# Kernel tuning notes

Hardware: AMD Instinct MI355X
Metric: run time of the kernel (lower is better)

The kernel has to match this reference:

```python
import jax, jax.numpy as jnp
import numpy as np

N = 100000
D = 64
FE = 8
E = 1600000


def setup_inputs() -> dict:
    key = jax.random.key(0)
    ks = jax.random.split(key, 24)
    s = 0.05
    inp = {
        "H_adapted_t": jax.random.normal(ks[0], (N, D), jnp.float32),
        "event_vector": jax.random.normal(ks[1], (N, FE), jnp.float32),
        "edge_index": jax.random.randint(ks[2], (2, E), 0, N, jnp.int32),
        # event encoder MLP
        "enc_W1": jax.random.normal(ks[3], (FE, D), jnp.float32) * s,
        "enc_b1": jnp.zeros((D,), jnp.float32),
        "enc_W2": jax.random.normal(ks[4], (D, D), jnp.float32) * s,
        "enc_b2": jnp.zeros((D,), jnp.float32),
        # GCNConv
        "gcn_W": jax.random.normal(ks[5], (D, D), jnp.float32) * s,
        "gcn_b": jnp.zeros((D,), jnp.float32),
        # GATConv (heads=1, concat=False)
        "gat_W": jax.random.normal(ks[6], (D, D), jnp.float32) * s,
        "gat_att_src": jax.random.normal(ks[7], (D,), jnp.float32) * s,
        "gat_att_dst": jax.random.normal(ks[8], (D,), jnp.float32) * s,
        "gat_b": jnp.zeros((D,), jnp.float32),
        # gate fusion
        "gate_W": jax.random.normal(ks[9], (2 * D, D), jnp.float32) * s,
        "gate_b": jnp.zeros((D,), jnp.float32),
        # residual decoder
        "res_W1": jax.random.normal(ks[10], (2 * D, D), jnp.float32) * s,
        "res_b1": jnp.zeros((D,), jnp.float32),
        "res_W2": jax.random.normal(ks[11], (D, D), jnp.float32) * s,
        "res_b2": jnp.zeros((D,), jnp.float32),
        # speed head
        "sp_W1": jax.random.normal(ks[12], (D, 32), jnp.float32) * s,
        "sp_b1": jnp.zeros((32,), jnp.float32),
        "sp_W2": jax.random.normal(ks[13], (32, 1), jnp.float32) * s,
        "sp_b2": jnp.zeros((1,), jnp.float32),
    }
    return inp


def _gcn(x, src, dst, W, b, n):
    # PyG GCNConv: x' = D^{-1/2} (A + I) D^{-1/2} X W + b
    h = x @ W
    deg = jax.ops.segment_sum(jnp.ones_like(dst, jnp.float32), dst, num_segments=n)
    dinv = jnp.where(deg > 0, jax.lax.rsqrt(jnp.maximum(deg, 1e-12)), 0.0)
    norm = dinv[src] * dinv[dst]  # [E+N]
    out = jax.ops.segment_sum(h[src] * norm[:, None], dst, num_segments=n)
    return out + b


def _gat(x, src, dst, W, att_src, att_dst, b, n):
    # PyG GATConv (1 head): alpha = softmax_dst(leaky_relu(a_s.Wx_src + a_d.Wx_dst))
    h = x @ W
    a_s = h @ att_src  # [n]
    a_d = h @ att_dst
    e = jax.nn.leaky_relu(a_s[src] + a_d[dst], negative_slope=0.2)  # [E+N]
    m = jax.ops.segment_max(e, dst, num_segments=n)
    ex = jnp.exp(e - m[dst])
    z = jax.ops.segment_sum(ex, dst, num_segments=n)
    alpha = ex / z[dst]
    out = jax.ops.segment_sum(h[src] * alpha[:, None], dst, num_segments=n)
    return out + b


def reference(H_adapted_t, event_vector, edge_index,
              enc_W1, enc_b1, enc_W2, enc_b2,
              gcn_W, gcn_b,
              gat_W, gat_att_src, gat_att_dst, gat_b,
              gate_W, gate_b,
              res_W1, res_b1, res_W2, res_b2,
              sp_W1, sp_b1, sp_W2, sp_b2):
    n = H_adapted_t.shape[0]
    # add self-loops (PyG default for both convs)
    loop = jnp.arange(n, dtype=edge_index.dtype)
    src = jnp.concatenate([edge_index[0], loop])
    dst = jnp.concatenate([edge_index[1], loop])

    # event encoder
    emb = jax.nn.relu(event_vector @ enc_W1 + enc_b1) @ enc_W2 + enc_b2
    # diffusion: GCN -> ReLU -> GAT -> ReLU
    x = jax.nn.relu(_gcn(emb, src, dst, gcn_W, gcn_b, n))
    diffused = jax.nn.relu(_gat(x, src, dst, gat_W, gat_att_src, gat_att_dst, gat_b, n))

    fusion = jnp.concatenate([H_adapted_t, diffused], axis=-1)  # [N, 2D]
    gate = jax.nn.sigmoid(fusion @ gate_W + gate_b)
    delta_raw = jax.nn.relu(fusion @ res_W1 + res_b1) @ res_W2 + res_b2
    delta = gate * delta_raw
    H_final = H_adapted_t + delta
    pred_speed = (jax.nn.relu(H_final @ sp_W1 + sp_b1) @ sp_W2 + sp_b2)[:, 0]
    return (delta, H_final, pred_speed)
```

## Files before the change

### kernel.cpp

```cpp
#include <hip/hip_runtime.h>
#include <hip/hip_bf16.h>

#define NN 100000
#define DD 64
#define FEE 8
#define EE 1600000

#define NBUCK 391
#define BCAP 6144
#define CHA 4096
#define NBLKA ((EE + CHA - 1) / CHA)

typedef __attribute__((ext_vector_type(8))) short bf16x8;
typedef __attribute__((ext_vector_type(4))) float f32x4;
typedef __attribute__((ext_vector_type(2))) float f32x2;

__device__ __forceinline__ float b2f(unsigned short u) {
    return __uint_as_float(((unsigned)u) << 16);
}
__device__ __forceinline__ unsigned short f2b(float f) {
    unsigned u = __float_as_uint(f);
    unsigned r = 0x7fffu + ((u >> 16) & 1u);
    return (unsigned short)((u + r) >> 16);
}
__device__ __forceinline__ float lrelu(float v) { return v > 0.f ? v : 0.2f * v; }
__device__ __forceinline__ unsigned fkey(float x) {
    unsigned b = __float_as_uint(x);
    return (b & 0x80000000u) ? ~b : (b | 0x80000000u);
}
__device__ __forceinline__ float funkey(unsigned u) {
    unsigned b = (u & 0x80000000u) ? (u & 0x7fffffffu) : ~u;
    return __uint_as_float(b);
}
__device__ __forceinline__ int rdlane(int v, int l) {
    return __builtin_amdgcn_readlane(v, l);
}
__device__ __forceinline__ float rdlanef(float v, int l) {
    return __int_as_float(__builtin_amdgcn_readlane(__float_as_int(v), l));
}
__device__ __forceinline__ bf16x8 pack8(const float* p) {
    const float4 a = *(const float4*)p;
    const float4 b = *(const float4*)(p + 4);
    bf16x8 r;
    r[0] = (short)f2b(a.x); r[1] = (short)f2b(a.y);
    r[2] = (short)f2b(a.z); r[3] = (short)f2b(a.w);
    r[4] = (short)f2b(b.x); r[5] = (short)f2b(b.y);
    r[6] = (short)f2b(b.z); r[7] = (short)f2b(b.w);
    return r;
}

__device__ __forceinline__ float deq8(unsigned v) {
#if __has_builtin(__builtin_amdgcn_cvt_f32_fp8)
    return __builtin_amdgcn_cvt_f32_fp8(v & 0xffu, 0);
#else
    unsigned t = v & 0x7fu;
    float m = __uint_as_float(0x3C000000u + (t << 20));
    if (t < 8) m = 2.f * m - 0.015625f;
    return (v & 0x80u) ? -m : m;
#endif
}
__device__ __forceinline__ float4 deq8x4(unsigned v) {
#if __has_builtin(__builtin_amdgcn_cvt_pk_f32_fp8)
    f32x2 lo = __builtin_amdgcn_cvt_pk_f32_fp8((int)v, false);
    f32x2 hi = __builtin_amdgcn_cvt_pk_f32_fp8((int)v, true);
    return make_float4(lo[0], lo[1], hi[0], hi[1]);
#else
    return make_float4(deq8(v), deq8(v >> 8), deq8(v >> 16), deq8(v >> 24));
#endif
}
__device__ __forceinline__ unsigned q8(float f) {
    unsigned u = __float_as_uint(f);
    unsigned s = (u >> 24) & 0x80u;
    float a = fminf(__uint_as_float(u & 0x7fffffffu), 448.f);
    unsigned t;
    if (a < 0.015625f) {
        t = (unsigned)__float2int_rn(a * 512.f);
    } else {
        unsigned b = __float_as_uint(a);
        b += ((b >> 20) & 1u) + 0x7FFFFu;
        unsigned e = (b >> 23) - 120u;
        t = (e > 15u) ? 0x7Eu : (((b >> 20) & 7u) | (e << 3));
    }
    return s | t;
}
__device__ __forceinline__ unsigned pk4(float a, float b, float c, float d) {
    return q8(a) | (q8(b) << 8) | (q8(c) << 16) | (q8(d) << 24);
}

#define LK 136
#define LK2 72

__global__ __launch_bounds__(256, 4) void k_encoder_mfma(
    const float* __restrict__ ev, const float* __restrict__ W1, const float* __restrict__ b1,
    const float* __restrict__ W2, const float* __restrict__ b2,
    const float* __restrict__ gcnW, const float* __restrict__ dinv,
    unsigned char* __restrict__ hA8)
{
    __shared__ short sW1T[64 * 32];
    __shared__ short sW2T[64 * LK2];
    __shared__ short sGWT[64 * LK2];
    __shared__ float sb1[64], sb2[64];
    __shared__ short sStage[4][16 * LK2];

    for (int t = threadIdx.x; t < 64 * 32; t += 256) {
        int n = t >> 5, k = t & 31;
        sW1T[n * 32 + k] = (k < FEE) ? (short)f2b(W1[k * 64 + n]) : (short)0;
    }
    for (int t = threadIdx.x; t < 64 * 64; t += 256) {
        int k = t >> 6, n = t & 63;
        sW2T[n * LK2 + k] = (short)f2b(W2[t]);
        sGWT[n * LK2 + k] = (short)f2b(gcnW[t]);
    }
    if (threadIdx.x < 64) {
        sb1[threadIdx.x] = b1[threadIdx.x];
        sb2[threadIdx.x] = b2[threadIdx.x];
    }
    __syncthreads();

    const int wave = threadIdx.x >> 6;
    const int lane = threadIdx.x & 63;
    const int m16  = lane & 15;
    const int quad = lane >> 4;
    short* myStage = &sStage[wave][0];

    const int ngroups = NN / 16;
    for (int g = blockIdx.x * 4 + wave; g < ngroups; g += gridDim.x * 4) {
        const int row0 = g * 16;
        bf16x8 a0;
        #pragma unroll
        for (int i = 0; i < 8; i++) a0[i] = 0;
        if (quad == 0) a0 = pack8(ev + (size_t)(row0 + m16) * FEE);
        f32x4 acc[4];
        #pragma unroll
        for (int c = 0; c < 4; c++) {
            f32x4 z = {0.f, 0.f, 0.f, 0.f};
            acc[c] = __builtin_amdgcn_mfma_f32_16x16x32_bf16(
                a0, *(const bf16x8*)&sW1T[(c * 16 + m16) * 32 + quad * 8], z, 0, 0, 0);
        }
        #pragma unroll
        for (int c = 0; c < 4; c++) {
            int n = c * 16 + m16;
            float bb = sb1[n];
            #pragma unroll
            for (int r = 0; r < 4; r++)
                myStage[(quad * 4 + r) * LK2 + n] = (short)f2b(fmaxf(acc[c][r] + bb, 0.f));
        }
        bf16x8 af0 = *(const bf16x8*)&myStage[m16 * LK2 + quad * 8];
        bf16x8 af1 = *(const bf16x8*)&myStage[m16 * LK2 + 32 + quad * 8];
        #pragma unroll
        for (int c = 0; c < 4; c++) {
            f32x4 z = {0.f, 0.f, 0.f, 0.f};
            const short* bp = &sW2T[(c * 16 + m16) * LK2 + quad * 8];
            z = __builtin_amdgcn_mfma_f32_16x16x32_bf16(af0, *(const bf16x8*)bp, z, 0, 0, 0);
            acc[c] = __builtin_amdgcn_mfma_f32_16x16x32_bf16(af1, *(const bf16x8*)(bp + 32), z, 0, 0, 0);
        }
        #pragma unroll
        for (int c = 0; c < 4; c++) {
            int n = c * 16 + m16;
            float bb = sb2[n];
            #pragma unroll
            for (int r = 0; r < 4; r++)
                myStage[(quad * 4 + r) * LK2 + n] = (short)f2b(acc[c][r] + bb);
        }
        af0 = *(const bf16x8*)&myStage[m16 * LK2 + quad * 8];
        af1 = *(const bf16x8*)&myStage[m16 * LK2 + 32 + quad * 8];
        #pragma unroll
        for (int c = 0; c < 4; c++) {
            f32x4 z = {0.f, 0.f, 0.f, 0.f};
            const short* bp = &sGWT[(c * 16 + m16) * LK2 + quad * 8];
            z = __builtin_amdgcn_mfma_f32_16x16x32_bf16(af0, *(const bf16x8*)bp, z, 0, 0, 0);
            acc[c] = __builtin_amdgcn_mfma_f32_16x16x32_bf16(af1, *(const bf16x8*)(bp + 32), z, 0, 0, 0);
        }
        #pragma unroll
        for (int c = 0; c < 4; c++) {
            int n = c * 16 + m16;
            #pragma unroll
            for (int r = 0; r < 4; r++)
                myStage[(quad * 4 + r) * LK2 + n] = (short)f2b(acc[c][r]);
        }
        #pragma unroll
        for (int h = 0; h < 2; h++) {
            int row = h * 8 + (lane >> 3);
            int col = (lane & 7) * 8;
            float sc = 32.f * dinv[row0 + row];
            const short* sp = &myStage[row * LK2 + col];
            uint2 w;
            w.x = pk4(b2f(sp[0]) * sc, b2f(sp[1]) * sc, b2f(sp[2]) * sc, b2f(sp[3]) * sc);
            w.y = pk4(b2f(sp[4]) * sc, b2f(sp[5]) * sc, b2f(sp[6]) * sc, b2f(sp[7]) * sc);
            *(uint2*)(hA8 + (size_t)(row0 + row) * 64 + col) = w;
        }
    }
}

__global__ __launch_bounds__(256, 4) void k_gatw_mfma(
    const unsigned short* __restrict__ x, const float* __restrict__ gatW,
    const float* __restrict__ attS, const float* __restrict__ attD,
    unsigned char* __restrict__ hC8, float* __restrict__ a_s, float* __restrict__ a_d)
{
    __shared__ short sGWT[64 * LK2];
    __shared__ float sAS[64], sAD[64];
    __shared__ short sStage[4][16 * LK2];
    for (int t = threadIdx.x; t < 64 * 64; t += 256) {
        int k = t >> 6, n = t & 63;
        sGWT[n * LK2 + k] = (short)f2b(gatW[t]);
    }
    if (threadIdx.x < 64) {
        sAS[threadIdx.x] = attS[threadIdx.x];
        sAD[threadIdx.x] = attD[threadIdx.x];
    }
    __syncthreads();

    const int wave = threadIdx.x >> 6;
    const int lane = threadIdx.x & 63;
    const int m16  = lane & 15;
    const int quad = lane >> 4;
    short* myStage = &sStage[wave][0];

    const int ngroups = NN / 16;
    for (int g = blockIdx.x * 4 + wave; g < ngroups; g += gridDim.x * 4) {
        const int row0 = g * 16;
        const unsigned short* xr = x + (size_t)(row0 + m16) * 64 + quad * 8;
        bf16x8 af0 = *(const bf16x8*)xr;
        bf16x8 af1 = *(const bf16x8*)(xr + 32);
        f32x4 acc[4];
        #pragma unroll
        for (int c = 0; c < 4; c++) {
            f32x4 z = {0.f, 0.f, 0.f, 0.f};
            const short* bp = &sGWT[(c * 16 + m16) * LK2 + quad * 8];
            z = __builtin_amdgcn_mfma_f32_16x16x32_bf16(af0, *(const bf16x8*)bp, z, 0, 0, 0);
            acc[c] = __builtin_amdgcn_mfma_f32_16x16x32_bf16(af1, *(const bf16x8*)(bp + 32), z, 0, 0, 0);
        }
        float ps[4] = {0.f, 0.f, 0.f, 0.f}, pd[4] = {0.f, 0.f, 0.f, 0.f};
        #pragma unroll
        for (int c = 0; c < 4; c++) {
            int n = c * 16 + m16;
            float was = sAS[n], wad = sAD[n];
            #pragma unroll
            for (int r = 0; r < 4; r++) {
                float v = acc[c][r];
                myStage[(quad * 4 + r) * LK2 + n] = (short)f2b(v);
                ps[r] += v * was;
                pd[r] += v * wad;
            }
        }
        #pragma unroll
        for (int off = 1; off < 16; off <<= 1) {
            #pragma unroll
            for (int r = 0; r < 4; r++) {
                ps[r] += __shfl_xor(ps[r], off, 64);
                pd[r] += __shfl_xor(pd[r], off, 64);
            }
        }
        if (m16 == 0) {
            #pragma unroll
            for (int r = 0; r < 4; r++) {
                a_s[row0 + quad * 4 + r] = ps[r];
                a_d[row0 + quad * 4 + r] = pd[r];
            }
        }
        #pragma unroll
        for (int h = 0; h < 2; h++) {
            int row = h * 8 + (lane >> 3);
            int col = (lane & 7) * 8;
            const short* sp = &myStage[row * LK2 + col];
            uint2 w;
            w.x = pk4(b2f(sp[0]) * 32.f, b2f(sp[1]) * 32.f, b2f(sp[2]) * 32.f, b2f(sp[3]) * 32.f);
            w.y = pk4(b2f(sp[4]) * 32.f, b2f(sp[5]) * 32.f, b2f(sp[6]) * 32.f, b2f(sp[7]) * 32.f);
            *(uint2*)(hC8 + (size_t)(row0 + row) * 64 + col) = w;
        }
    }
}

__global__ __launch_bounds__(512, 4) void k_decoder_mfma(
    const float* __restrict__ H, const float* diff,
    const float* __restrict__ gateW, const float* __restrict__ gateB,
    const float* __restrict__ resW1, const float* __restrict__ resB1,
    const float* __restrict__ resW2, const float* __restrict__ resB2,
    const float* __restrict__ spW1, const float* __restrict__ spB1,
    const float* __restrict__ spW2, const float* __restrict__ spB2,
    float* outDelta, float* __restrict__ outH, float* __restrict__ outP)
{
    __shared__ short sGW[64 * LK];
    __shared__ short sRW1[64 * LK];
    __shared__ short sRW2[64 * LK2];
    __shared__ short sSW1[32 * LK2];
    __shared__ float sGB[64], sRB1[64], sRB2[64];
    __shared__ float sSB1[32], sSW2[32];
    __shared__ float sSB2;
    __shared__ short sStage[8][16 * LK2];

    for (int t = threadIdx.x; t < 128 * 64; t += 512) {
        int k = t >> 6, n = t & 63;
        sGW[n * LK + k]  = (short)f2b(gateW[t]);
        sRW1[n * LK + k] = (short)f2b(resW1[t]);
    }
    for (int t = threadIdx.x; t < 64 * 64; t += 512) {
        int k = t >> 6, n = t & 63;
        sRW2[n * LK2 + k] = (short)f2b(resW2[t]);
    }
    for (int t = threadIdx.x; t < 64 * 32; t += 512) {
        int k = t >> 5, n = t & 31;
        sSW1[n * LK2 + k] = (short)f2b(spW1[t]);
    }
    if (threadIdx.x < 64) {
        sGB[threadIdx.x]  = gateB[threadIdx.x];
        sRB1[threadIdx.x] = resB1[threadIdx.x];
        sRB2[threadIdx.x] = resB2[threadIdx.x];
    }
    if (threadIdx.x < 32) {
        sSB1[threadIdx.x] = spB1[threadIdx.x];
        sSW2[threadIdx.x] = spW2[threadIdx.x];
    }
    if (threadIdx.x == 0) sSB2 = spB2[0];
    __syncthreads();

    const int wave = threadIdx.x >> 6;
    const int lane = threadIdx.x & 63;
    const int m16  = lane & 15;
    const int quad = lane >> 4;
    short* myStage = &sStage[wave][0];

    const int ngroups = NN / 16;
    for (int g = blockIdx.x * 8 + wave; g < ngroups; g += gridDim.x * 8) {
        const int row0 = g * 16;
        const float* Hrow = H    + (size_t)(row0 + m16) * 64 + quad * 8;
        const float* Drow = diff + (size_t)(row0 + m16) * 64 + quad * 8;
        bf16x8 afrag[4];
        afrag[0] = pack8(Hrow);
        afrag[1] = pack8(Hrow + 32);
        afrag[2] = pack8(Drow);
        afrag[3] = pack8(Drow + 32);

        f32x4 accG[4], accR[4];
        #pragma unroll
        for (int c = 0; c < 4; c++) {
            f32x4 z = {0.f, 0.f, 0.f, 0.f};
            accG[c] = z; accR[c] = z;
        }
        #pragma unroll
        for (int c = 0; c < 4; c++) {
            const short* bg = &sGW[(c * 16 + m16) * LK + quad * 8];
            const short* br = &sRW1[(c * 16 + m16) * LK + quad * 8];
            #pragma unroll
            for (int t = 0; t < 4; t++) {
                bf16x8 bgf = *(const bf16x8*)(bg + 32 * t);
                accG[c] = __builtin_amdgcn_mfma_f32_16x16x32_bf16(afrag[t], bgf, accG[c], 0, 0, 0);
                bf16x8 brf = *(const bf16x8*)(br + 32 * t);
                accR[c] = __builtin_amdgcn_mfma_f32_16x16x32_bf16(afrag[t], brf, accR[c], 0, 0, 0);
            }
        }

        float gateV[4][4];
        #pragma unroll
        for (int c = 0; c < 4; c++) {
            int n = c * 16 + m16;
            float gb = sGB[n], rb = sRB1[n];
            #pragma unroll
            for (int r = 0; r < 4; r++) {
                gateV[c][r] = 1.f / (1.f + __expf(-(accG[c][r] + gb)));
                int mrow = quad * 4 + r;
                myStage[mrow * LK2 + n] = (short)f2b(fmaxf(accR[c][r] + rb, 0.f));
            }
        }
        bf16x8 h1f0 = *(const bf16x8*)&myStage[m16 * LK2 + quad * 8];
        bf16x8 h1f1 = *(const bf16x8*)&myStage[m16 * LK2 + 32 + quad * 8];

        f32x4 accD[4];
        #pragma unroll
        for (int c = 0; c < 4; c++) { f32x4 z = {0.f, 0.f, 0.f, 0.f}; accD[c] = z; }
        #pragma unroll
        for (int c = 0; c < 4; c++) {
            const short* bp = &sRW2[(c * 16 + m16) * LK2 + quad * 8];
            accD[c] = __builtin_amdgcn_mfma_f32_16x16x32_bf16(h1f0, *(const bf16x8*)bp, accD[c], 0, 0, 0);
            accD[c] = __builtin_amdgcn_mfma_f32_16x16x32_bf16(h1f1, *(const bf16x8*)(bp + 32), accD[c], 0, 0, 0);
        }

        #pragma unroll
        for (int c = 0; c < 4; c++) {
            int n = c * 16 + m16;
            float rb2 = sRB2[n];
            #pragma unroll
            for (int r = 0; r < 4; r++) {
                int mrow = quad * 4 + r;
                float delta = gateV[c][r] * (accD[c][r] + rb2);
                float hv = H[(size_t)(row0 + mrow) * 64 + n];
                float hf = hv + delta;
                outDelta[(size_t)(row0 + mrow) * 64 + n] = delta;
                outH[(size_t)(row0 + mrow) * 64 + n] = hf;
                myStage[mrow * LK2 + n] = (short)f2b(hf);
            }
        }
        bf16x8 hff0 = *(const bf16x8*)&myStage[m16 * LK2 + quad * 8];
        bf16x8 hff1 = *(const bf16x8*)&myStage[m16 * LK2 + 32 + quad * 8];

        f32x4 accS[2];
        { f32x4 z = {0.f, 0.f, 0.f, 0.f}; accS[0] = z; accS[1] = z; }
        #pragma unroll
        for (int c = 0; c < 2; c++) {
            const short* bp = &sSW1[(c * 16 + m16) * LK2 + quad * 8];
            accS[c] = __builtin_amdgcn_mfma_f32_16x16x32_bf16(hff0, *(const bf16x8*)bp, accS[c], 0, 0, 0);
            accS[c] = __builtin_amdgcn_mfma_f32_16x16x32_bf16(hff1, *(const bf16x8*)(bp + 32), accS[c], 0, 0, 0);
        }
        float part[4];
        #pragma unroll
        for (int r = 0; r < 4; r++) {
            float p0 = fmaxf(accS[0][r] + sSB1[m16], 0.f) * sSW2[m16];
            float p1 = fmaxf(accS[1][r] + sSB1[16 + m16], 0.f) * sSW2[16 + m16];
            part[r] = p0 + p1;
        }
        #pragma unroll
        for (int off = 1; off < 16; off <<= 1) {
            #pragma unroll
            for (int r = 0; r < 4; r++) part[r] += __shfl_xor(part[r], off, 64);
        }
        if (m16 == 0) {
            #pragma unroll
            for (int r = 0; r < 4; r++) outP[row0 + quad * 4 + r] = part[r] + sSB2;
        }
    }
}


__global__ __launch_bounds__(256, 2) void k_binA(
    const int* __restrict__ src, const int* __restrict__ dst,
    int* __restrict__ bcnt, int* __restrict__ bpacked)
{
    __shared__ int sCount[512];
    __shared__ int sOff[512];
    __shared__ int sCur[512];
    __shared__ int sGbase[512];
    __shared__ int sScan[256];
    __shared__ int sStage[CHA];
    __shared__ unsigned short sBkt[CHA];
    const int t = threadIdx.x;
    const int e0 = blockIdx.x * CHA;
    const int len = min(CHA, EE - e0);

    for (int i = t; i < 512; i += 256) sCount[i] = 0;
    __syncthreads();
    for (int i = t; i < len; i += 256) atomicAdd(&sCount[dst[e0 + i] >> 8], 1);
    __syncthreads();
    int a0 = sCount[2 * t], a1 = sCount[2 * t + 1];
    int pairsum = a0 + a1;
    sScan[t] = pairsum;
    __syncthreads();
    for (int off = 1; off < 256; off <<= 1) {
        int v = (t >= off) ? sScan[t - off] : 0;
        __syncthreads();
        sScan[t] += v;
        __syncthreads();
    }
    int excl = sScan[t] - pairsum;
    sOff[2 * t] = excl;       sOff[2 * t + 1] = excl + a0;
    sCur[2 * t] = excl;       sCur[2 * t + 1] = excl + a0;
    __syncthreads();
    for (int b = t; b < NBUCK; b += 256) {
        int c = sCount[b];
        sGbase[b] = c ? atomicAdd(&bcnt[b], c) : 0;
    }
    __syncthreads();
    for (int i = t; i < len; i += 256) {
        int d = dst[e0 + i];
        int s = src[e0 + i];
        int b = d >> 8;
        int p = atomicAdd(&sCur[b], 1);
        sStage[p] = ((d & 255) << 17) | s;
        sBkt[p] = (unsigned short)b;
    }
    __syncthreads();
    for (int i = t; i < len; i += 256) {
        int b = sBkt[i];
        int gp = sGbase[b] + (i - sOff[b]);
        if (gp < BCAP) bpacked[(size_t)b * BCAP + gp] = sStage[i];
    }
}

__global__ __launch_bounds__(256) void k_fillB2(
    const int* __restrict__ bcnt, const int* __restrict__ bpacked,
    int* __restrict__ row_ptr, int* __restrict__ rend, float* __restrict__ dinv,
    int* __restrict__ csr)
{
    __shared__ int lcnt[256];
    __shared__ int lscan[256];
    __shared__ int lcur[256];
    __shared__ int lstage[BCAP];
    __shared__ int sWs[4];
    __shared__ int sBase;
    const int b = blockIdx.x;
    const int t = threadIdx.x;
    const int node0 = b << 8;
    const int cnt = min(bcnt[b], BCAP);
    lcnt[t] = 0;
    int partial = 0;
    for (int i = t; i < b; i += 256) partial += bcnt[i];
    #pragma unroll
    for (int o = 32; o >= 1; o >>= 1) partial += __shfl_xor(partial, o, 64);
    if ((t & 63) == 0) sWs[t >> 6] = partial;
    __syncthreads();
    if (t == 0) sBase = sWs[0] + sWs[1] + sWs[2] + sWs[3];
    const int* bp = bpacked + (size_t)b * BCAP;
    for (int i = t; i < cnt; i += 256) atomicAdd(&lcnt[bp[i] >> 17], 1);
    __syncthreads();
    const int base = sBase;
    int own = lcnt[t];
    lscan[t] = own;
    __syncthreads();
    for (int off = 1; off < 256; off <<= 1) {
        int v = (t >= off) ? lscan[t - off] : 0;
        __syncthreads();
        lscan[t] += v;
        __syncthreads();
    }
    int excl = lscan[t] - own;
    int node = node0 + t;
    if (node < NN) {
        row_ptr[node] = base + excl;
        rend[node] = base + excl + own;
        dinv[node] = rsqrtf((float)own + 1.0f);
    }
    lcur[t] = excl;
    __syncthreads();
    for (int i = t; i < cnt; i += 256) {
        int v = bp[i];
        int p = atomicAdd(&lcur[v >> 17], 1);
        lstage[p] = v & 0x1FFFF;
    }
    __syncthreads();
    for (int i = t; i < cnt; i += 256) csr[base + i] = lstage[i];
}


__global__ __launch_bounds__(256) void k_gcn_gather(
    const int* __restrict__ row_ptr, const int* __restrict__ rend,
    const int* __restrict__ csr, const float* __restrict__ dinv,
    const unsigned char* __restrict__ hA8, const float* __restrict__ gcnB,
    unsigned short* __restrict__ x)
{
    const int slot = threadIdx.x >> 6;
    const int lane = threadIdx.x & 63;
    const int g    = lane >> 4;
    const int c4   = (lane & 15) * 4;
    const float4 gb = *(const float4*)(gcnB + c4);
    const int stride = gridDim.x * 4;
    for (int node = blockIdx.x * 4 + slot; node < NN; node += stride) {
        const int base = row_ptr[node], end = rend[node];
        float r0 = 0.f, r1 = 0.f, r2 = 0.f, r3 = 0.f;
        for (int cb = base; cb < end; cb += 64) {
            int rem = end - cb; if (rem > 64) rem = 64;
            int sidx = (lane < rem) ? csr[cb + lane] : 0;
            int k = 0;
            for (; k + 16 <= rem; k += 16) {
                #pragma unroll
                for (int u = 0; u < 4; u++) {
                    int s = __shfl(sidx, k + u * 4 + g, 64);
                    unsigned v = *(const unsigned*)(hA8 + (((unsigned)s << 6) | (unsigned)c4));
                    float4 d = deq8x4(v);
                    r0 += d.x; r1 += d.y; r2 += d.z; r3 += d.w;
                }
            }
            for (; k < rem; k += 4) {
                int kk = k + g;
                int kc = min(kk, rem - 1);
                int s = __shfl(sidx, kc, 64);
                float w = (kk < rem) ? 1.f : 0.f;
                unsigned v = *(const unsigned*)(hA8 + (((unsigned)s << 6) | (unsigned)c4));
                float4 d = deq8x4(v);
                r0 = fmaf(d.x, w, r0); r1 = fmaf(d.y, w, r1);
                r2 = fmaf(d.z, w, r2); r3 = fmaf(d.w, w, r3);
            }
        }
        r0 += __shfl_xor(r0, 16, 64); r0 += __shfl_xor(r0, 32, 64);
        r1 += __shfl_xor(r1, 16, 64); r1 += __shfl_xor(r1, 32, 64);
        r2 += __shfl_xor(r2, 16, 64); r2 += __shfl_xor(r2, 32, 64);
        r3 += __shfl_xor(r3, 16, 64); r3 += __shfl_xor(r3, 32, 64);
        unsigned sv = *(const unsigned*)(hA8 + (((unsigned)node << 6) | (unsigned)c4));
        float4 sd = deq8x4(sv);
        float sc = dinv[node] * 0.03125f;
        if (g == 0) {
            float o0 = fmaxf(fmaf(r0 + sd.x, sc, gb.x), 0.f);
            float o1 = fmaxf(fmaf(r1 + sd.y, sc, gb.y), 0.f);
            float o2 = fmaxf(fmaf(r2 + sd.z, sc, gb.z), 0.f);
            float o3 = fmaxf(fmaf(r3 + sd.w, sc, gb.w), 0.f);
            uint2 wv;
            wv.x = (unsigned)f2b(o0) | ((unsigned)f2b(o1) << 16);
            wv.y = (unsigned)f2b(o2) | ((unsigned)f2b(o3) << 16);
            *(uint2*)(x + (size_t)node * 64 + c4) = wv;
        }
    }
}

__global__ __launch_bounds__(256) void k_gat_fused(
    const int* __restrict__ row_ptr, const int* __restrict__ rend,
    const int* __restrict__ csr,
    const float* __restrict__ a_s, const float* __restrict__ a_d,
    const unsigned char* __restrict__ hC8, const float* __restrict__ gatB,
    float* __restrict__ diff)
{
    const int slot = threadIdx.x >> 6;
    const int lane = threadIdx.x & 63;
    const int g    = lane >> 4;
    const int c4   = (lane & 15) * 4;
    const float4 gb = *(const float4*)(gatB + c4);
    const int stride = gridDim.x * 4;
    for (int node = blockIdx.x * 4 + slot; node < NN; node += stride) {
        const int base = row_ptr[node], end = rend[node];
        const float adn = a_d[node];
        const float p0 = __expf(lrelu(a_s[node] + adn));
        float z = p0;
        float r0 = 0.f, r1 = 0.f, r2 = 0.f, r3 = 0.f;
        for (int cb = base; cb < end; cb += 64) {
            int rem = end - cb; if (rem > 64) rem = 64;
            int sidx = 0; float p = 0.f;
            if (lane < rem) {
                sidx = csr[cb + lane];
                p = __expf(lrelu(a_s[sidx] + adn));
            }
            float pzs = p;
            #pragma unroll
            for (int o = 32; o >= 1; o >>= 1) pzs += __shfl_xor(pzs, o, 64);
            z += pzs;
            int k = 0;
            for (; k + 16 <= rem; k += 16) {
                #pragma unroll
                for (int u = 0; u < 4; u++) {
                    int kk = k + u * 4 + g;
                    int s = __shfl(sidx, kk, 64);
                    float w = __shfl(p, kk, 64);
                    unsigned v = *(const unsigned*)(hC8 + (((unsigned)s << 6) | (unsigned)c4));
                    float4 d = deq8x4(v);
                    r0 = fmaf(d.x, w, r0); r1 = fmaf(d.y, w, r1);
                    r2 = fmaf(d.z, w, r2); r3 = fmaf(d.w, w, r3);
                }
            }
            for (; k < rem; k += 4) {
                int kk = k + g;
                int kc = min(kk, rem - 1);
                int s = __shfl(sidx, kc, 64);
                float w = __shfl(p, kc, 64);
                if (kk >= rem) w = 0.f;
                unsigned v = *(const unsigned*)(hC8 + (((unsigned)s << 6) | (unsigned)c4));
                float4 d = deq8x4(v);
                r0 = fmaf(d.x, w, r0); r1 = fmaf(d.y, w, r1);
                r2 = fmaf(d.z, w, r2); r3 = fmaf(d.w, w, r3);
            }
        }
        r0 += __shfl_xor(r0, 16, 64); r0 += __shfl_xor(r0, 32, 64);
        r1 += __shfl_xor(r1, 16, 64); r1 += __shfl_xor(r1, 32, 64);
        r2 += __shfl_xor(r2, 16, 64); r2 += __shfl_xor(r2, 32, 64);
        r3 += __shfl_xor(r3, 16, 64); r3 += __shfl_xor(r3, 32, 64);
        unsigned sv = *(const unsigned*)(hC8 + (((unsigned)node << 6) | (unsigned)c4));
        float4 sd = deq8x4(sv);
        r0 = fmaf(sd.x, p0, r0); r1 = fmaf(sd.y, p0, r1);
        r2 = fmaf(sd.z, p0, r2); r3 = fmaf(sd.w, p0, r3);
        if (g == 0) {
            float inv = 1.f / (32.f * z);
            float4 ov;
            ov.x = fmaxf(fmaf(r0, inv, gb.x), 0.f);
            ov.y = fmaxf(fmaf(r1, inv, gb.y), 0.f);
            ov.z = fmaxf(fmaf(r2, inv, gb.z), 0.f);
            ov.w = fmaxf(fmaf(r3, inv, gb.w), 0.f);
            *(float4*)(diff + (size_t)node * 64 + c4) = ov;
        }
    }
}


__global__ __launch_bounds__(256, 4) void k_encoder(
    const float* __restrict__ ev, const float* __restrict__ W1, const float* __restrict__ b1,
    const float* __restrict__ W2, const float* __restrict__ b2,
    const float* __restrict__ gcnW, unsigned short* __restrict__ hA)
{
    __shared__ float sW1[FEE * DD];
    __shared__ float sW2[DD * DD];
    __shared__ float sGW[DD * DD];
    __shared__ float sb1[DD], sb2[DD];
    __shared__ float stage[4 * DD];
    for (int t = threadIdx.x; t < FEE * DD; t += 256) sW1[t] = W1[t];
    for (int t = threadIdx.x; t < DD * DD; t += 256) sW2[t] = W2[t];
    for (int t = threadIdx.x; t < DD * DD; t += 256) sGW[t] = gcnW[t];
    if (threadIdx.x < DD) {
        sb1[threadIdx.x] = b1[threadIdx.x];
        sb2[threadIdx.x] = b2[threadIdx.x];
    }
    __syncthreads();
    const int slot = threadIdx.x >> 6, j = threadIdx.x & 63;
    const int ngroups = NN / 4;
    for (int g = blockIdx.x; g < ngroups; g += gridDim.x) {
        int node = g * 4 + slot;
        const float* evp = ev + node * FEE;
        float accv = sb1[j];
        #pragma unroll
        for (int i = 0; i < FEE; i++) accv += evp[i] * sW1[i * DD + j];
        float hid = fmaxf(accv, 0.f);
        stage[slot * DD + j] = hid;
        __syncthreads();
        float embv = sb2[j];
        #pragma unroll 8
        for (int i = 0; i < DD; i++) embv += stage[slot * DD + i] * sW2[i * DD + j];
        __syncthreads();
        stage[slot * DD + j] = embv;
        __syncthreads();
        float hv = 0.f;
        #pragma unroll 8
        for (int i = 0; i < DD; i++) hv += stage[slot * DD + i] * sGW[i * DD + j];
        hA[node * DD + j] = f2b(hv);
        __syncthreads();
    }
}

__global__ void k_degf(const int* __restrict__ dst, float* __restrict__ deg) {
    int e = blockIdx.x * 256 + threadIdx.x;
    if (e < EE) atomicAdd(&deg[dst[e]], 1.0f);
}
__global__ void k_dinvf(float* deg) {
    int i = blockIdx.x * 256 + threadIdx.x;
    if (i < NN) deg[i] = rsqrtf(deg[i] + 1.0f);
}
__global__ __launch_bounds__(256) void k_gcn_agg(
    const int* __restrict__ src, const int* __restrict__ dst,
    const float* __restrict__ dinv, const unsigned short* __restrict__ hA,
    float* __restrict__ acc)
{
    int lane = threadIdx.x & 63;
    int w = blockIdx.x * 4 + (threadIdx.x >> 6);
    int nw = gridDim.x * 4;
    for (int e = w; e < EE; e += nw) {
        int s = src[e], d = dst[e];
        float norm = dinv[s] * dinv[d];
        atomicAdd(&acc[d * DD + lane], b2f(hA[s * DD + lane]) * norm);
    }
}
__global__ __launch_bounds__(256, 4) void k_gcn_post(
    const float* __restrict__ acc, const unsigned short* __restrict__ hA,
    const float* __restrict__ dinv, const float* __restrict__ gcnB,
    const float* __restrict__ gatW, const float* __restrict__ attS, const float* __restrict__ attD,
    unsigned short* __restrict__ hC, float* __restrict__ a_s, float* __restrict__ a_d,
    unsigned int* __restrict__ mkey)
{
    __shared__ float sGW[DD * DD];
    __shared__ float sB[DD], sAS[DD], sAD[DD];
    __shared__ float stage[4 * DD];
    for (int t = threadIdx.x; t < DD * DD; t += 256) sGW[t] = gatW[t];
    if (threadIdx.x < DD) {
        sB[threadIdx.x] = gcnB[threadIdx.x];
        sAS[threadIdx.x] = attS[threadIdx.x];
        sAD[threadIdx.x] = attD[threadIdx.x];
    }
    __syncthreads();
    const int slot = threadIdx.x >> 6, j = threadIdx.x & 63;
    const int ngroups = NN / 4;
    for (int g = blockIdx.x; g < ngroups; g += gridDim.x) {
        int node = g * 4 + slot;
        float dv = dinv[node];
        float xv = fmaxf(acc[node * DD + j] + b2f(hA[node * DD + j]) * dv * dv + sB[j], 0.f);
        stage[slot * DD + j] = xv;
        __syncthreads();
        float hv = 0.f;
        #pragma unroll 8
        for (int i = 0; i < DD; i++) hv += stage[slot * DD + i] * sGW[i * DD + j];
        hC[node * DD + j] = f2b(hv);
        float ts = hv * sAS[j], td = hv * sAD[j];
        #pragma unroll
        for (int m = 32; m >= 1; m >>= 1) {
            ts += __shfl_xor(ts, m, 64);
            td += __shfl_xor(td, m, 64);
        }
        if (j == 0) {
            a_s[node] = ts;
            a_d[node] = td;
            mkey[node] = fkey(lrelu(ts + td));
        }
        __syncthreads();
    }
}
__global__ void k_gat_max(const int* __restrict__ src, const int* __restrict__ dst,
                          const float* __restrict__ a_s, const float* __restrict__ a_d,
                          unsigned int* __restrict__ mkey) {
    int e = blockIdx.x * 256 + threadIdx.x;
    if (e < EE) {
        int d = dst[e];
        float v = lrelu(a_s[src[e]] + a_d[d]);
        atomicMax(&mkey[d], fkey(v));
    }
}
__global__ void k_gat_mz(const float* __restrict__ a_s, const float* __restrict__ a_d,
                         unsigned int* __restrict__ mkey, float* __restrict__ z) {
    int i = blockIdx.x * 256 + threadIdx.x;
    if (i < NN) {
        float m = funkey(mkey[i]);
        float es = lrelu(a_s[i] + a_d[i]);
        z[i] = expf(es - m);
        ((float*)mkey)[i] = m;
    }
}
__global__ void k_gat_z(const int* __restrict__ src, const int* __restrict__ dst,
                        const float* __restrict__ a_s, const float* __restrict__ a_d,
                        const float* __restrict__ mf, float* __restrict__ z) {
    int e = blockIdx.x * 256 + threadIdx.x;
    if (e < EE) {
        int d = dst[e];
        float v = lrelu(a_s[src[e]] + a_d[d]);
        atomicAdd(&z[d], expf(v - mf[d]));
    }
}
__global__ __launch_bounds__(256) void k_gat_agg(
    const int* __restrict__ src, const int* __restrict__ dst,
    const float* __restrict__ a_s, const float* __restrict__ a_d,
    const float* __restrict__ mf, const float* __restrict__ z,
    const unsigned short* __restrict__ hC, float* __restrict__ acc)
{
    int lane = threadIdx.x & 63;
    int w = blockIdx.x * 4 + (threadIdx.x >> 6);
    int nw = gridDim.x * 4;
    for (int e = w; e < EE; e += nw) {
        int s = src[e], d = dst[e];
        float v = lrelu(a_s[s] + a_d[d]);
        float alpha = expf(v - mf[d]) / z[d];
        atomicAdd(&acc[d * DD + lane], b2f(hC[s * DD + lane]) * alpha);
    }
}
__global__ void k_gat_post(float* __restrict__ acc, const unsigned short* __restrict__ hC,
                           const float* __restrict__ a_s, const float* __restrict__ a_d,
                           const float* __restrict__ mf, const float* __restrict__ z,
                           const float* __restrict__ gatB) {
    int idx = blockIdx.x * 256 + threadIdx.x;
    if (idx < NN * DD) {
        int i = idx >> 6, j = idx & 63;
        float es = lrelu(a_s[i] + a_d[i]);
        float sw = expf(es - mf[i]) / z[i];
        float v = acc[idx] + sw * b2f(hC[idx]) + gatB[j];
        acc[idx] = fmaxf(v, 0.f);
    }
}


extern "C" void kernel_launch(void* const* d_in, const int* in_sizes, int n_in,
                              void* d_out, int out_size, void* d_ws, size_t ws_size,
                              hipStream_t stream) {
    const float* H     = (const float*)d_in[0];
    const float* ev    = (const float*)d_in[1];
    const int*   ei    = (const int*)d_in[2];
    const float* encW1 = (const float*)d_in[3];
    const float* encB1 = (const float*)d_in[4];
    const float* encW2 = (const float*)d_in[5];
    const float* encB2 = (const float*)d_in[6];
    const float* gcnW  = (const float*)d_in[7];
    const float* gcnB  = (const float*)d_in[8];
    const float* gatW  = (const float*)d_in[9];
    const float* attS  = (const float*)d_in[10];
    const float* attD  = (const float*)d_in[11];
    const float* gatB  = (const float*)d_in[12];
    const float* gateW = (const float*)d_in[13];
    const float* gateB = (const float*)d_in[14];
    const float* resW1 = (const float*)d_in[15];
    const float* resB1 = (const float*)d_in[16];
    const float* resW2 = (const float*)d_in[17];
    const float* resB2 = (const float*)d_in[18];
    const float* spW1  = (const float*)d_in[19];
    const float* spB1  = (const float*)d_in[20];
    const float* spW2  = (const float*)d_in[21];
    const float* spB2  = (const float*)d_in[22];

    const int* srcI = ei;
    const int* dstI = ei + EE;

    float* outDelta = (float*)d_out;
    float* outH     = outDelta + (size_t)NN * DD;
    float* outP     = outH + (size_t)NN * DD;

    float* diff = outDelta;
    int* bpacked = (int*)outDelta;
    unsigned short* x   = (unsigned short*)outDelta;
    unsigned char* hA8  = (unsigned char*)outH;
    unsigned char* hC8  = hA8 + (size_t)NN * DD;

    const size_t csr_need = ((size_t)4 * NN + EE + 1024) * 4;

    if (ws_size >= csr_need) {
        float* dinv = (float*)d_ws;
        float* a_s  = dinv + NN;
        float* a_d  = a_s + NN;
        int* rend   = (int*)(a_d + NN);
        int* csr    = rend + NN;
        int* bcntg  = csr + EE;
        int* row_ptr = (int*)outP;

        hipMemsetAsync(bcntg, 0, (size_t)512 * 4, stream);
        k_binA<<<NBLKA, 256, 0, stream>>>(srcI, dstI, bcntg, bpacked);
        k_fillB2<<<NBUCK, 256, 0, stream>>>(bcntg, bpacked,
                                            row_ptr, rend, dinv, csr);
        k_encoder_mfma<<<1024, 256, 0, stream>>>(ev, encW1, encB1, encW2, encB2,
                                                 gcnW, dinv, hA8);
        k_gcn_gather<<<4096, 256, 0, stream>>>(row_ptr, rend, csr, dinv, hA8, gcnB, x);
        k_gatw_mfma<<<1024, 256, 0, stream>>>(x, gatW, attS, attD, hC8, a_s, a_d);
        k_gat_fused<<<4096, 256, 0, stream>>>(row_ptr, rend, csr, a_s, a_d, hC8, gatB, diff);
    } else {
        float* dinv = (float*)d_ws;
        float* a_s  = dinv + NN;
        float* a_d  = a_s + NN;
        float* mf   = a_d + NN;
        float* z    = mf + NN;
        float* acc  = diff;
        unsigned short* hA = (unsigned short*)outH;
        unsigned short* hC = hA + (size_t)NN * DD;

        hipMemsetAsync(dinv, 0, (size_t)NN * 4, stream);
        hipMemsetAsync(acc, 0, (size_t)NN * DD * 4, stream);
        k_encoder<<<1024, 256, 0, stream>>>(ev, encW1, encB1, encW2, encB2, gcnW, hA);
        k_degf<<<(EE + 255) / 256, 256, 0, stream>>>(dstI, dinv);
        k_dinvf<<<(NN + 255) / 256, 256, 0, stream>>>(dinv);
        k_gcn_agg<<<8192, 256, 0, stream>>>(srcI, dstI, dinv, hA, acc);
        k_gcn_post<<<1024, 256, 0, stream>>>(acc, hA, dinv, gcnB, gatW, attS, attD,
                                             hC, a_s, a_d, (unsigned int*)mf);
        hipMemsetAsync(acc, 0, (size_t)NN * DD * 4, stream);
        k_gat_max<<<(EE + 255) / 256, 256, 0, stream>>>(srcI, dstI, a_s, a_d, (unsigned int*)mf);
        k_gat_mz<<<(NN + 255) / 256, 256, 0, stream>>>(a_s, a_d, (unsigned int*)mf, z);
        k_gat_z<<<(EE + 255) / 256, 256, 0, stream>>>(srcI, dstI, a_s, a_d, mf, z);
        k_gat_agg<<<8192, 256, 0, stream>>>(srcI, dstI, a_s, a_d, mf, z, hC, acc);
        k_gat_post<<<(NN * DD) / 256, 256, 0, stream>>>(acc, hC, a_s, a_d, mf, z, gatB);
    }

    k_decoder_mfma<<<512, 512, 0, stream>>>(H, diff, gateW, gateB, resW1, resB1,
                                            resW2, resB2, spW1, spB1, spW2, spB2,
                                            outDelta, outH, outP);
}
```

Measured before the change: 284.6 us.

## Process two nodes per wave in GCN/GAT gathers with LDS-staged edge lists

Each 64-lane wave now handles two destination nodes, one per 32-lane half, instead of one node across four 16-lane groups. Edge source indices and weights are staged in per-half shared memory rather than broadcast with shuffles. The gather loop first issues 8 independent row loads, then dequantizes and accumulates them, to raise memory-level parallelism. The cost is more registers and LDS traffic, plus unsynchronized LDS reuse within a half-wave, which relies on wave-lockstep execution.

Result: faster. 262.0 us (-7.9%).

```diff
diff --git a/kernel.cpp b/kernel.cpp
--- a/kernel.cpp
+++ b/kernel.cpp
@@ -31,12 +31,6 @@
 __device__ __forceinline__ float funkey(unsigned u) {
     unsigned b = (u & 0x80000000u) ? (u & 0x7fffffffu) : ~u;
     return __uint_as_float(b);
-}
-__device__ __forceinline__ int rdlane(int v, int l) {
-    return __builtin_amdgcn_readlane(v, l);
-}
-__device__ __forceinline__ float rdlanef(float v, int l) {
-    return __int_as_float(__builtin_amdgcn_readlane(__float_as_int(v), l));
 }
 __device__ __forceinline__ bf16x8 pack8(const float* p) {
     const float4 a = *(const float4*)p;
@@ -536,47 +530,62 @@
     const unsigned char* __restrict__ hA8, const float* __restrict__ gcnB,
     unsigned short* __restrict__ x)
 {
-    const int slot = threadIdx.x >> 6;
+    __shared__ int2 sE[4][2][32];
+    const int wave = threadIdx.x >> 6;
     const int lane = threadIdx.x & 63;
-    const int g    = lane >> 4;
+    const int half = lane >> 5;
+    const int hl   = lane & 31;
+    const int g2   = hl >> 4;
     const int c4   = (lane & 15) * 4;
+    int2* myE = sE[wave][half];
     const float4 gb = *(const float4*)(gcnB + c4);
-    const int stride = gridDim.x * 4;
-    for (int node = blockIdx.x * 4 + slot; node < NN; node += stride) {
+    const int stride = gridDim.x * 8;
+    for (int node = blockIdx.x * 8 + wave * 2 + half; node < NN; node += stride) {
         const int base = row_ptr[node], end = rend[node];
         float r0 = 0.f, r1 = 0.f, r2 = 0.f, r3 = 0.f;
-        for (int cb = base; cb < end; cb += 64) {
-            int rem = end - cb; if (rem > 64) rem = 64;
-            int sidx = (lane < rem) ? csr[cb + lane] : 0;
+        for (int cb = base; cb < end; cb += 32) {
+            int rem = end - cb; if (rem > 32) rem = 32;
+            int sidx = 0; float w = 0.f;
+            if (hl < rem) { sidx = csr[cb + hl]; w = 1.f; }
+            myE[hl] = make_int2(sidx, __float_as_int(w));
             int k = 0;
             for (; k + 16 <= rem; k += 16) {
+                unsigned vv[8]; float ww[8];
                 #pragma unroll
-                for (int u = 0; u < 4; u++) {
-                    int s = __shfl(sidx, k + u * 4 + g, 64);
-                    unsigned v = *(const unsigned*)(hA8 + (((unsigned)s << 6) | (unsigned)c4));
-                    float4 d = deq8x4(v);
-                    r0 += d.x; r1 += d.y; r2 += d.z; r3 += d.w;
+                for (int j = 0; j < 8; j++) {
+                    int2 e = myE[k + 2 * j + g2];
+                    ww[j] = __int_as_float(e.y);
+                    vv[j] = *(const unsigned*)(hA8 + (((unsigned)e.x << 6) | (unsigned)c4));
                 }
-            }
-            for (; k < rem; k += 4) {
-                int kk = k + g;
-                int kc = min(kk, rem - 1);
-                int s = __shfl(sidx, kc, 64);
-                float w = (kk < rem) ? 1.f : 0.f;
-                unsigned v = *(const unsigned*)(hA8 + (((unsigned)s << 6) | (unsigned)c4));
-                float4 d = deq8x4(v);
-                r0 = fmaf(d.x, w, r0); r1 = fmaf(d.y, w, r1);
-                r2 = fmaf(d.z, w, r2); r3 = fmaf(d.w, w, r3);
-            }
-        }
-        r0 += __shfl_xor(r0, 16, 64); r0 += __shfl_xor(r0, 32, 64);
-        r1 += __shfl_xor(r1, 16, 64); r1 += __shfl_xor(r1, 32, 64);
-        r2 += __shfl_xor(r2, 16, 64); r2 += __shfl_xor(r2, 32, 64);
-        r3 += __shfl_xor(r3, 16, 64); r3 += __shfl_xor(r3, 32, 64);
+                #pragma unroll
+                for (int j = 0; j < 8; j++) {
+                    float4 d = deq8x4(vv[j]);
+                    r0 = fmaf(d.x, ww[j], r0); r1 = fmaf(d.y, ww[j], r1);
+                    r2 = fmaf(d.z, ww[j], r2); r3 = fmaf(d.w, ww[j], r3);
+                }
+            }
+            for (; k < rem; k += 8) {
+                unsigned vv[4]; float ww[4];
+                #pragma unroll
+                for (int j = 0; j < 4; j++) {
+                    int2 e = myE[k + 2 * j + g2];
+                    ww[j] = __int_as_float(e.y);
+                    vv[j] = *(const unsigned*)(hA8 + (((unsigned)e.x << 6) | (unsigned)c4));
+                }
+                #pragma unroll
+                for (int j = 0; j < 4; j++) {
+                    float4 d = deq8x4(vv[j]);
+                    r0 = fmaf(d.x, ww[j], r0); r1 = fmaf(d.y, ww[j], r1);
+                    r2 = fmaf(d.z, ww[j], r2); r3 = fmaf(d.w, ww[j], r3);
+                }
+            }
+        }
+        r0 += __shfl_xor(r0, 16, 64); r1 += __shfl_xor(r1, 16, 64);
+        r2 += __shfl_xor(r2, 16, 64); r3 += __shfl_xor(r3, 16, 64);
         unsigned sv = *(const unsigned*)(hA8 + (((unsigned)node << 6) | (unsigned)c4));
         float4 sd = deq8x4(sv);
         float sc = dinv[node] * 0.03125f;
-        if (g == 0) {
+        if (g2 == 0) {
             float o0 = fmaxf(fmaf(r0 + sd.x, sc, gb.x), 0.f);
             float o1 = fmaxf(fmaf(r1 + sd.y, sc, gb.y), 0.f);
             float o2 = fmaxf(fmaf(r2 + sd.z, sc, gb.z), 0.f);
@@ -596,63 +605,73 @@
     const unsigned char* __restrict__ hC8, const float* __restrict__ gatB,
     float* __restrict__ diff)
 {
-    const int slot = threadIdx.x >> 6;
+    __shared__ int2 sE[4][2][32];
+    const int wave = threadIdx.x >> 6;
     const int lane = threadIdx.x & 63;
-    const int g    = lane >> 4;
+    const int half = lane >> 5;
+    const int hl   = lane & 31;
+    const int g2   = hl >> 4;
     const int c4   = (lane & 15) * 4;
+    int2* myE = sE[wave][half];
     const float4 gb = *(const float4*)(gatB + c4);
-    const int stride = gridDim.x * 4;
-    for (int node = blockIdx.x * 4 + slot; node < NN; node += stride) {
+    const int stride = gridDim.x * 8;
+    for (int node = blockIdx.x * 8 + wave * 2 + half; node < NN; node += stride) {
         const int base = row_ptr[node], end = rend[node];
         const float adn = a_d[node];
         const float p0 = __expf(lrelu(a_s[node] + adn));
-        float z = p0;
+        float zl = 0.f;
         float r0 = 0.f, r1 = 0.f, r2 = 0.f, r3 = 0.f;
-        for (int cb = base; cb < end; cb += 64) {
-            int rem = end - cb; if (rem > 64) rem = 64;
+        for (int cb = base; cb < end; cb += 32) {
+            int rem = end - cb; if (rem > 32) rem = 32;
             int sidx = 0; float p = 0.f;
-            if (lane < rem) {
-                sidx = csr[cb + lane];
+            if (hl < rem) {
+                sidx = csr[cb + hl];
                 p = __expf(lrelu(a_s[sidx] + adn));
             }
-            float pzs = p;
-            #pragma unroll
-            for (int o = 32; o >= 1; o >>= 1) pzs += __shfl_xor(pzs, o, 64);
-            z += pzs;
+            myE[hl] = make_int2(sidx, __float_as_int(p));
+            zl += p;
             int k = 0;
             for (; k + 16 <= rem; k += 16) {
+                unsigned vv[8]; float ww[8];
                 #pragma unroll
-                for (int u = 0; u < 4; u++) {
-                    int kk = k + u * 4 + g;
-                    int s = __shfl(sidx, kk, 64);
-                    float w = __shfl(p, kk, 64);
-                    unsigned v = *(const unsigned*)(hC8 + (((unsigned)s << 6) | (unsigned)c4));
-                    float4 d = deq8x4(v);
-                    r0 = fmaf(d.x, w, r0); r1 = fmaf(d.y, w, r1);
-                    r2 = fmaf(d.z, w, r2); r3 = fmaf(d.w, w, r3);
+                for (int j = 0; j < 8; j++) {
+                    int2 e = myE[k + 2 * j + g2];
+                    ww[j] = __int_as_float(e.y);
+                    vv[j] = *(const unsigned*)(hC8 + (((unsigned)e.x << 6) | (unsigned)c4));
                 }
-            }
-            for (; k < rem; k += 4) {
-                int kk = k + g;
-                int kc = min(kk, rem - 1);
-                int s = __shfl(sidx, kc, 64);
-                float w = __shfl(p, kc, 64);
-                if (kk >= rem) w = 0.f;
-                unsigned v = *(const unsigned*)(hC8 + (((unsigned)s << 6) | (unsigned)c4));
-                float4 d = deq8x4(v);
-                r0 = fmaf(d.x, w, r0); r1 = fmaf(d.y, w, r1);
-                r2 = fmaf(d.z, w, r2); r3 = fmaf(d.w, w, r3);
-            }
-        }
-        r0 += __shfl_xor(r0, 16, 64); r0 += __shfl_xor(r0, 32, 64);
-        r1 += __shfl_xor(r1, 16, 64); r1 += __shfl_xor(r1, 32, 64);
-        r2 += __shfl_xor(r2, 16, 64); r2 += __shfl_xor(r2, 32, 64);
-        r3 += __shfl_xor(r3, 16, 64); r3 += __shfl_xor(r3, 32, 64);
+                #pragma unroll
+                for (int j = 0; j < 8; j++) {
+                    float4 d = deq8x4(vv[j]);
+                    r0 = fmaf(d.x, ww[j], r0); r1 = fmaf(d.y, ww[j], r1);
+                    r2 = fmaf(d.z, ww[j], r2); r3 = fmaf(d.w, ww[j], r3);
+                }
+            }
+            for (; k < rem; k += 8) {
+                unsigned vv[4]; float ww[4];
+                #pragma unroll
+                for (int j = 0; j < 4; j++) {
+                    int2 e = myE[k + 2 * j + g2];
+                    ww[j] = __int_as_float(e.y);
+                    vv[j] = *(const unsigned*)(hC8 + (((unsigned)e.x << 6) | (unsigned)c4));
+                }
+                #pragma unroll
+                for (int j = 0; j < 4; j++) {
+                    float4 d = deq8x4(vv[j]);
+                    r0 = fmaf(d.x, ww[j], r0); r1 = fmaf(d.y, ww[j], r1);
+                    r2 = fmaf(d.z, ww[j], r2); r3 = fmaf(d.w, ww[j], r3);
+                }
+            }
+        }
+        #pragma unroll
+        for (int o = 16; o >= 1; o >>= 1) zl += __shfl_xor(zl, o, 64);
+        float z = p0 + zl;
+        r0 += __shfl_xor(r0, 16, 64); r1 += __shfl_xor(r1, 16, 64);
+        r2 += __shfl_xor(r2, 16, 64); r3 += __shfl_xor(r3, 16, 64);
         unsigned sv = *(const unsigned*)(hC8 + (((unsigned)node << 6) | (unsigned)c4));
         float4 sd = deq8x4(sv);
         r0 = fmaf(sd.x, p0, r0); r1 = fmaf(sd.y, p0, r1);
         r2 = fmaf(sd.z, p0, r2); r3 = fmaf(sd.w, p0, r3);
-        if (g == 0) {
+        if (g2 == 0) {
             float inv = 1.f / (32.f * z);
             float4 ov;
             ov.x = fmaxf(fmaf(r0, inv, gb.x), 0.f);
```
